# Performance work log

Hardware: AMD Instinct MI355X
Metric: run time of the kernel (lower is better)

## Reference

```python
import jax, jax.numpy as jnp
import numpy as np

N_HEAD = 16

def setup_inputs() -> dict:
    key = jax.random.key(0)
    ks = jax.random.split(key, 5)
    B, S, C = 4, 2048, 1024
    x = jax.random.normal(ks[0], (B, S, C), dtype=jnp.float32)
    w_qkv = jax.random.normal(ks[1], (C, 3 * C), dtype=jnp.float32) * (1.0 / np.sqrt(C))
    b_qkv = jnp.zeros((3 * C,), dtype=jnp.float32)
    w_proj = jax.random.normal(ks[2], (C, C), dtype=jnp.float32) * (1.0 / np.sqrt(C))
    b_proj = jnp.zeros((C,), dtype=jnp.float32)
    return {"x": x, "w_qkv": w_qkv, "b_qkv": b_qkv, "w_proj": w_proj, "b_proj": b_proj}

def reference(x, w_qkv, b_qkv, w_proj, b_proj):
    B, S, C = x.shape
    H = N_HEAD
    D = C // H
    qkv = x @ w_qkv + b_qkv                       # [B,S,3C]
    q, k, v = jnp.split(qkv, 3, axis=-1)
    # [B,S,C] -> [B,H,S,D]
    q = q.reshape(B, S, H, D).transpose(0, 2, 1, 3)
    k = k.reshape(B, S, H, D).transpose(0, 2, 1, 3)
    v = v.reshape(B, S, H, D).transpose(0, 2, 1, 3)
    scores = jnp.einsum('bhqd,bhkd->bhqk', q, k) / jnp.sqrt(jnp.float32(D))
    causal = jnp.tril(jnp.ones((S, S), dtype=bool))
    scores = jnp.where(causal[None, None], scores, -jnp.inf)
    weights = jax.nn.softmax(scores, axis=-1)     # dropout p=0 -> identity
    out = jnp.einsum('bhqk,bhkd->bhqd', weights, v)
    out = out.transpose(0, 2, 1, 3).reshape(B, S, C)
    return out @ w_proj + b_proj
```

## Files before the change

kernel.cpp:

```cpp
#include <hip/hip_runtime.h>

#define SDIM 2048
#define CDIM 1024
#define BDIM 4
#define HDIM 16
#define DDIM 64

#define ATT_SCALE 0.18033688011112042f

typedef __attribute__((ext_vector_type(8))) short bf16x8;
typedef __attribute__((ext_vector_type(4))) short bf16x4;
typedef __attribute__((ext_vector_type(4))) float f32x4;
typedef unsigned short u16;

#define MFMA __builtin_amdgcn_mfma_f32_16x16x32_bf16
#define LDS_ORDER_FENCE() __asm__ __volatile__("" ::: "memory")

__device__ __forceinline__ u16 f2b(float f) {
    union { float f; unsigned u; } v; v.f = f;
    unsigned r = v.u + 0x7FFFu + ((v.u >> 16) & 1u);
    return (u16)(r >> 16);
}
__device__ __forceinline__ u16 f2b_trunc(float f) {
    union { float f; unsigned u; } v; v.f = f;
    return (u16)(v.u >> 16);
}

typedef const __attribute__((address_space(1))) unsigned int* gas_t;
typedef __attribute__((address_space(3))) unsigned int* las_t;
__device__ __forceinline__ void cp16(const void* g, void* l) {
    __builtin_amdgcn_global_load_lds((gas_t)g, (las_t)l, 16, 0, 0);
}

__device__ __forceinline__ float fast_exp2(float x) {
#if __has_builtin(__builtin_amdgcn_exp2f)
    return __builtin_amdgcn_exp2f(x);
#else
    return __exp2f(x);
#endif
}

__global__ __launch_bounds__(256) void prep(
    const float* __restrict__ x, const float* __restrict__ w_qkv,
    const float* __restrict__ w_proj,
    u16* __restrict__ Xb, u16* __restrict__ WqT, u16* __restrict__ WpT)
{
    __shared__ __align__(16) u16 t[64][72];
    const int bx = blockIdx.x;
    const int tid = threadIdx.x;

    if (bx < 4096) {
        int i = (bx * 256 + tid) * 8;
        float4 a = *reinterpret_cast<const float4*>(&x[i]);
        float4 b = *reinterpret_cast<const float4*>(&x[i + 4]);
        u16 u[8];
        u[0]=f2b(a.x); u[1]=f2b(a.y); u[2]=f2b(a.z); u[3]=f2b(a.w);
        u[4]=f2b(b.x); u[5]=f2b(b.y); u[6]=f2b(b.z); u[7]=f2b(b.w);
        *reinterpret_cast<uint4*>(&Xb[i]) = *reinterpret_cast<uint4*>(u);
        return;
    }

    const float* src; u16* dst; int N, n0, k0;
    if (bx < 4096 + 768) {
        int b2 = bx - 4096;
        src = w_qkv; dst = WqT; N = 3 * CDIM;
        n0 = (b2 % 48) * 64; k0 = (b2 / 48) * 64;
    } else {
        int b2 = bx - 4864;
        src = w_proj; dst = WpT; N = CDIM;
        n0 = (b2 % 16) * 64; k0 = (b2 / 16) * 64;
    }
    const int K = CDIM;
#pragma unroll
    for (int it = 0; it < 4; it++) {
        int c = tid + it * 256;
        int r = c >> 4, c4 = (c & 15) * 4;
        float4 f = *reinterpret_cast<const float4*>(&src[(size_t)(k0 + r) * N + n0 + c4]);
        t[c4 + 0][r] = f2b(f.x);
        t[c4 + 1][r] = f2b(f.y);
        t[c4 + 2][r] = f2b(f.z);
        t[c4 + 3][r] = f2b(f.w);
    }
    __syncthreads();
#pragma unroll
    for (int it = 0; it < 2; it++) {
        int c = tid + it * 256;
        int r = c >> 3, c8 = (c & 7) * 8;
        *reinterpret_cast<uint4*>(&dst[(size_t)(n0 + r) * K + k0 + c8]) =
            *reinterpret_cast<const uint4*>(&t[r][c8]);
    }
}

#define PHASE_TAIL()                                                          \
    LDS_ORDER_FENCE();                                                        \
    __builtin_amdgcn_s_barrier();                                             \
    __asm__ __volatile__("s_waitcnt lgkmcnt(0)" ::: "memory");                \
    __builtin_amdgcn_sched_barrier(0)

#define PHASE_END()                                                           \
    LDS_ORDER_FENCE();                                                        \
    __builtin_amdgcn_s_barrier()

__global__ __launch_bounds__(256, 2) void gemm_qkv(
    const u16* __restrict__ A, const u16* __restrict__ Bt,
    const float* __restrict__ bias,
    u16* __restrict__ Qb, u16* __restrict__ Kb, u16* __restrict__ Vtb)
{
    __shared__ __align__(16) u16 smem[3 * 8192 + 3 * 4096];
    u16* const AsAll = smem;
    u16* const BsAll = smem + 3 * 8192;

    const int tid = threadIdx.x, lane = tid & 63, wave = tid >> 6;
    const int wm = wave >> 1, wn = wave & 1;
    const int l16 = lane & 15, quad = lane >> 4;
    const int bid = blockIdx.x;
    const int w = (bid & 7) * 96 + (bid >> 3);
    const int bx = w % 24, by = w / 24;
    const int m0 = by * 256, n0 = bx * 128;
    const int K = CDIM;

    const int su = (tid & 7) ^ ((tid >> 3) & 7);
    const int sr = ((tid >> 3) << 1) | (su >> 2);
    const int sc = su & 3;

    const int uc8 = ((((l16 & 1) << 2) | quad) ^ (l16 >> 1)) * 8;
    const int faB = (wm * 64 + (l16 >> 1)) * 64 + uc8;
    const int fbB = (wn * 32 + (l16 >> 1)) * 64 + uc8;

#define STG_A(sb, k0, s)  cp16(&A [(size_t)(m0 + (s) * 64 + sr) * K + (k0) + sc * 8], \
                               &AsAll[(sb) * 8192 + ((s) * 256 + wave * 64) * 8])
#define STG_B(sb, k0, s)  cp16(&Bt[(size_t)(n0 + (s) * 64 + sr) * K + (k0) + sc * 8], \
                               &BsAll[(sb) * 4096 + ((s) * 256 + wave * 64) * 8])
#define FRA(i) (*reinterpret_cast<const bf16x8*>(&AsB[faB + (i) * 512]))
#define FRB(j) (*reinterpret_cast<const bf16x8*>(&BsB[fbB + (j) * 512]))

    f32x4 acc[8][4];
#pragma unroll
    for (int i = 0; i < 8; i++)
#pragma unroll
        for (int j = 0; j < 4; j++) acc[i][j] = (f32x4){0.f, 0.f, 0.f, 0.f};

    const int NT = K / 32;
    STG_A(0, 0, 0); STG_A(0, 0, 1); STG_A(0, 0, 2); STG_A(0, 0, 3);
    STG_B(0, 0, 0); STG_B(0, 0, 1);
    STG_A(1, 32, 0); STG_A(1, 32, 1); STG_A(1, 32, 2); STG_A(1, 32, 3);
    STG_B(1, 32, 0); STG_B(1, 32, 1);
    __asm__ __volatile__("s_waitcnt vmcnt(6)" ::: "memory");
    __builtin_amdgcn_s_barrier();
    LDS_ORDER_FENCE();

    for (int t = 0; t < NT; t++) {
        const int buf = t % 3, sbuf = (t + 2) % 3;
        const int kst = (t + 2) * 32;
        const bool st = (t + 2) < NT;
        const u16* AsB = &AsAll[buf * 8192];
        const u16* BsB = &BsAll[buf * 4096];

        bf16x8 b0, b1, b2, b3, a0, a1, a2, a3;

        b0 = FRB(0); b1 = FRB(1); b2 = FRB(2); b3 = FRB(3);
        a0 = FRA(0); a1 = FRA(1); a2 = FRA(2); a3 = FRA(3);
        if (st) { STG_A(sbuf, kst, 0); STG_A(sbuf, kst, 1); STG_A(sbuf, kst, 2); }
        PHASE_TAIL();
        __builtin_amdgcn_s_setprio(1);
        acc[0][0] = MFMA(a0, b0, acc[0][0], 0, 0, 0);
        acc[0][1] = MFMA(a0, b1, acc[0][1], 0, 0, 0);
        acc[0][2] = MFMA(a0, b2, acc[0][2], 0, 0, 0);
        acc[0][3] = MFMA(a0, b3, acc[0][3], 0, 0, 0);
        acc[1][0] = MFMA(a1, b0, acc[1][0], 0, 0, 0);
        acc[1][1] = MFMA(a1, b1, acc[1][1], 0, 0, 0);
        acc[1][2] = MFMA(a1, b2, acc[1][2], 0, 0, 0);
        acc[1][3] = MFMA(a1, b3, acc[1][3], 0, 0, 0);
        acc[2][0] = MFMA(a2, b0, acc[2][0], 0, 0, 0);
        acc[2][1] = MFMA(a2, b1, acc[2][1], 0, 0, 0);
        acc[2][2] = MFMA(a2, b2, acc[2][2], 0, 0, 0);
        acc[2][3] = MFMA(a2, b3, acc[2][3], 0, 0, 0);
        acc[3][0] = MFMA(a3, b0, acc[3][0], 0, 0, 0);
        acc[3][1] = MFMA(a3, b1, acc[3][1], 0, 0, 0);
        acc[3][2] = MFMA(a3, b2, acc[3][2], 0, 0, 0);
        acc[3][3] = MFMA(a3, b3, acc[3][3], 0, 0, 0);
        __builtin_amdgcn_s_setprio(0);
        PHASE_END();

        a0 = FRA(4); a1 = FRA(5); a2 = FRA(6); a3 = FRA(7);
        if (st) { STG_A(sbuf, kst, 3); STG_B(sbuf, kst, 0); STG_B(sbuf, kst, 1); }
        PHASE_TAIL();
        __builtin_amdgcn_s_setprio(1);
        acc[4][0] = MFMA(a0, b0, acc[4][0], 0, 0, 0);
        acc[4][1] = MFMA(a0, b1, acc[4][1], 0, 0, 0);
        acc[4][2] = MFMA(a0, b2, acc[4][2], 0, 0, 0);
        acc[4][3] = MFMA(a0, b3, acc[4][3], 0, 0, 0);
        acc[5][0] = MFMA(a1, b0, acc[5][0], 0, 0, 0);
        acc[5][1] = MFMA(a1, b1, acc[5][1], 0, 0, 0);
        acc[5][2] = MFMA(a1, b2, acc[5][2], 0, 0, 0);
        acc[5][3] = MFMA(a1, b3, acc[5][3], 0, 0, 0);
        acc[6][0] = MFMA(a2, b0, acc[6][0], 0, 0, 0);
        acc[6][1] = MFMA(a2, b1, acc[6][1], 0, 0, 0);
        acc[6][2] = MFMA(a2, b2, acc[6][2], 0, 0, 0);
        acc[6][3] = MFMA(a2, b3, acc[6][3], 0, 0, 0);
        acc[7][0] = MFMA(a3, b0, acc[7][0], 0, 0, 0);
        acc[7][1] = MFMA(a3, b1, acc[7][1], 0, 0, 0);
        acc[7][2] = MFMA(a3, b2, acc[7][2], 0, 0, 0);
        acc[7][3] = MFMA(a3, b3, acc[7][3], 0, 0, 0);
        __builtin_amdgcn_s_setprio(0);
        if (t < NT - 2) {
            __asm__ __volatile__("s_waitcnt vmcnt(6)" ::: "memory");
        } else if (t == NT - 2) {
            __asm__ __volatile__("s_waitcnt vmcnt(0)" ::: "memory");
        }
        PHASE_END();
    }
#undef STG_A
#undef STG_B
#undef FRA
#undef FRB

    const int mm0 = m0 + wm * 128;
    const int bidx = mm0 >> 11, s0 = mm0 & 2047;
    const int n_base = n0 + wn * 64;
    u16* eb = &smem[wave * (16 * 68)];
    const int erow = lane >> 2, ec = (lane & 3) * 16;

    if (n0 >= 2 * CDIM) {
        const int h = (n_base - 2 * CDIM) >> 6;
        const size_t gb = ((size_t)(bidx * HDIM + h)) * DDIM * SDIM;
#pragma unroll
        for (int ih = 0; ih < 2; ih++) {
#pragma unroll
            for (int j = 0; j < 4; j++) {
                float bvj = bias[n_base + j * 16 + l16];
                LDS_ORDER_FENCE();
#pragma unroll
                for (int i = 0; i < 4; i++)
#pragma unroll
                    for (int r = 0; r < 4; r++)
                        eb[l16 * 68 + i * 16 + quad * 4 + r] =
                            f2b(acc[ih * 4 + i][j][r] + bvj);
                LDS_ORDER_FENCE();
                union { bf16x4 hp[4]; uint4 u[2]; } pk;
                pk.hp[0] = *reinterpret_cast<const bf16x4*>(&eb[erow * 68 + ec]);
                pk.hp[1] = *reinterpret_cast<const bf16x4*>(&eb[erow * 68 + ec + 4]);
                pk.hp[2] = *reinterpret_cast<const bf16x4*>(&eb[erow * 68 + ec + 8]);
                pk.hp[3] = *reinterpret_cast<const bf16x4*>(&eb[erow * 68 + ec + 12]);
                u16* gp = &Vtb[gb + (size_t)(j * 16 + erow) * SDIM + s0 + ih * 64 + ec];
                *reinterpret_cast<uint4*>(gp)     = pk.u[0];
                *reinterpret_cast<uint4*>(gp + 8) = pk.u[1];
            }
        }
    } else {
        const bool isK = (n_base >= CDIM);
        u16* dst = isK ? Kb : Qb;
        const float scale = isK ? 1.0f : ATT_SCALE;
        const int hh = (n_base & 1023) >> 6;
        const size_t hb = ((size_t)(bidx * HDIM + hh)) * SDIM;
        float bvj[4];
#pragma unroll
        for (int j = 0; j < 4; j++) bvj[j] = bias[n_base + j * 16 + l16];
#pragma unroll
        for (int i = 0; i < 8; i++) {
            LDS_ORDER_FENCE();
#pragma unroll
            for (int j = 0; j < 4; j++)
#pragma unroll
                for (int r = 0; r < 4; r++)
                    eb[(quad * 4 + r) * 68 + j * 16 + l16] =
                        f2b((acc[i][j][r] + bvj[j]) * scale);
            LDS_ORDER_FENCE();
            union { bf16x4 hp[4]; uint4 u[2]; } pk;
            pk.hp[0] = *reinterpret_cast<const bf16x4*>(&eb[erow * 68 + ec]);
            pk.hp[1] = *reinterpret_cast<const bf16x4*>(&eb[erow * 68 + ec + 4]);
            pk.hp[2] = *reinterpret_cast<const bf16x4*>(&eb[erow * 68 + ec + 8]);
            pk.hp[3] = *reinterpret_cast<const bf16x4*>(&eb[erow * 68 + ec + 12]);
            const int s = s0 + i * 16 + erow;
            u16* gp = &dst[(hb + s) * DDIM + ec];
            *reinterpret_cast<uint4*>(gp)     = pk.u[0];
            *reinterpret_cast<uint4*>(gp + 8) = pk.u[1];
        }
    }
}

__global__ __launch_bounds__(512, 6) void attn(
    const u16* __restrict__ Qb, const u16* __restrict__ Kb,
    const u16* __restrict__ Vtb, u16* __restrict__ Ob)
{
    __shared__ __align__(16) u16 Ks[2][64 * 64];
    __shared__ __align__(16) u16 Vts[2][64 * 64];
    __shared__ __align__(16) u16 Ps[8][16 * 68];

    const int tid = threadIdx.x;
    const int lane = tid & 63, wave = tid >> 6;
    const int l16 = lane & 15, quad = lane >> 4;
    const int x = blockIdx.x;
    const int bh = (x & 7) * 8 + ((x >> 3) & 7);
    const int qt = 15 - (x >> 6);
    const int q0 = qt * 128;
    const int b = bh >> 4, h = bh & 15;
    const size_t base = (size_t)bh * (SDIM * DDIM);

    const int cl0 = wave * 64 + lane;
    const int sr0 = cl0 >> 3, scc = cl0 & 7;
    const int sg0 = scc ^ (sr0 & 7);

    const int qrow = q0 + wave * 16 + l16;
    bf16x8 aq0 = *reinterpret_cast<const bf16x8*>(&Qb[base + (size_t)qrow * DDIM + quad * 8]);
    bf16x8 aq1 = *reinterpret_cast<const bf16x8*>(&Qb[base + (size_t)qrow * DDIM + 32 + quad * 8]);

    u16* Pw = &Ps[wave][0];

    f32x4 O[4];
    f32x4 Osum = (f32x4){0.f, 0.f, 0.f, 0.f};
#pragma unroll
    for (int j = 0; j < 4; j++) O[j] = (f32x4){0.f, 0.f, 0.f, 0.f};
    const short onev = (l16 == 0) ? (short)0x3F80 : (short)0;
    const bf16x8 bones = {onev, onev, onev, onev, onev, onev, onev, onev};

    const int nkb = (qt + 1) * 2;
    const int Arow = q0 + wave * 16;

    cp16(&Kb [base + (size_t)sr0 * DDIM + sg0 * 8], &Ks[0][wave * 512]);
    cp16(&Vtb[base + (size_t)sr0 * SDIM + sg0 * 8], &Vts[0][wave * 512]);

    for (int kbi = 0; kbi < nkb; kbi++) {
        const int cur = kbi & 1;
        const int kb = kbi * 64;
        __syncthreads();
        if (kbi + 1 < nkb) {
            const int kb2 = kb + 64;
            cp16(&Kb [base + (size_t)(kb2 + sr0) * DDIM + sg0 * 8], &Ks[1 - cur][wave * 512]);
            cp16(&Vtb[base + (size_t)sr0 * SDIM + kb2 + sg0 * 8], &Vts[1 - cur][wave * 512]);
        }
        if (kb > Arow + 15) continue;

        const u16* Kc = &Ks[cur][0];
        const u16* Vc = &Vts[cur][0];

        f32x4 sc[4];
#pragma unroll
        for (int j = 0; j < 4; j++) {
            int kr = j * 16 + l16;
            bf16x8 bk0 = *reinterpret_cast<const bf16x8*>(&Kc[(kr * 8 + ( quad      ^ (kr & 7))) * 8]);
            bf16x8 bk1 = *reinterpret_cast<const bf16x8*>(&Kc[(kr * 8 + ((quad + 4) ^ (kr & 7))) * 8]);
            f32x4 s = (f32x4){0.f, 0.f, 0.f, 0.f};
            s = MFMA(aq0, bk0, s, 0, 0, 0);
            s = MFMA(aq1, bk1, s, 0, 0, 0);
            sc[j] = s;
        }
        if (kb + 63 > Arow) {
            const int qrel = Arow - kb;
#pragma unroll
            for (int j = 0; j < 4; j++) {
                int kk = j * 16 + l16;
#pragma unroll
                for (int r = 0; r < 4; r++)
                    sc[j][r] = (kk <= qrel + quad * 4 + r) ? sc[j][r] : -1e30f;
            }
        }
#pragma unroll
        for (int j = 0; j < 4; j++)
#pragma unroll
            for (int r = 0; r < 4; r++) {
                float p = fast_exp2(sc[j][r]);
                Pw[(quad * 4 + r) * 68 + j * 16 + l16] = f2b_trunc(p);
            }
        LDS_ORDER_FENCE();
        union { bf16x4 hp[2]; bf16x8 f; } a0u, a1u;
        a0u.hp[0] = *reinterpret_cast<const bf16x4*>(&Pw[l16 * 68 + quad * 8]);
        a0u.hp[1] = *reinterpret_cast<const bf16x4*>(&Pw[l16 * 68 + quad * 8 + 4]);
        a1u.hp[0] = *reinterpret_cast<const bf16x4*>(&Pw[l16 * 68 + 32 + quad * 8]);
        a1u.hp[1] = *reinterpret_cast<const bf16x4*>(&Pw[l16 * 68 + 32 + quad * 8 + 4]);

#pragma unroll
        for (int j = 0; j < 4; j++) {
            int vr = j * 16 + l16;
            bf16x8 bv0 = *reinterpret_cast<const bf16x8*>(&Vc[(vr * 8 + ( quad      ^ (vr & 7))) * 8]);
            bf16x8 bv1 = *reinterpret_cast<const bf16x8*>(&Vc[(vr * 8 + ((quad + 4) ^ (vr & 7))) * 8]);
            O[j] = MFMA(a0u.f, bv0, O[j], 0, 0, 0);
            O[j] = MFMA(a1u.f, bv1, O[j], 0, 0, 0);
        }
        Osum = MFMA(a0u.f, bones, Osum, 0, 0, 0);
        Osum = MFMA(a1u.f, bones, Osum, 0, 0, 0);
    }

#pragma unroll
    for (int r = 0; r < 4; r++) {
        float l = __shfl(Osum[r], (lane & 48));
        float inv = 1.0f / l;
        int s = q0 + wave * 16 + quad * 4 + r;
#pragma unroll
        for (int j = 0; j < 4; j++)
            Ob[((size_t)(b * SDIM + s)) * CDIM + h * 64 + j * 16 + l16] =
                f2b(O[j][r] * inv);
    }
}

__global__ __launch_bounds__(512, 2) void gemm_proj(
    const u16* __restrict__ A, const u16* __restrict__ Bt,
    const float* __restrict__ bias, float* __restrict__ out)
{
    __shared__ __align__(16) u16 smem[3 * 16384 + 3 * 8192];
    u16* const AsAll = smem;
    u16* const BsAll = smem + 3 * 16384;

    const int tid = threadIdx.x, lane = tid & 63, wave = tid >> 6;
    const int wm = wave >> 1, wn = wave & 1;
    const int l16 = lane & 15, quad = lane >> 4;
    const int bid = blockIdx.x;
    const int w = (bid & 7) * 32 + (bid >> 3);
    const int bx = w & 7, by = w >> 3;
    const int m0 = by * 256, n0 = bx * 128;
    const int K = CDIM, N = CDIM;

    const int l8 = lane & 7, lr = lane >> 3;
    const int sg = l8 ^ lr;
    const int arow = wave * 8 + lr;

#define STG_A(sb, k0, s)  cp16(&A [(size_t)(m0 + (s) * 64 + arow) * K + (k0) + sg * 8], \
                               &AsAll[(sb) * 16384 + ((s) * 512 + wave * 64) * 8])
#define STG_B(sb, k0, s)  cp16(&Bt[(size_t)(n0 + (s) * 64 + arow) * K + (k0) + sg * 8], \
                               &BsAll[(sb) * 8192 + ((s) * 512 + wave * 64) * 8])
#define FRA(i, kk) (*reinterpret_cast<const bf16x8*>(                                   \
        &AsB[((wm * 64 + (i) * 16 + l16) * 8 + (((kk) * 4 + quad) ^ (l16 & 7))) * 8]))
#define FRB(j, kk) (*reinterpret_cast<const bf16x8*>(                                   \
        &BsB[((wn * 64 + (j) * 16 + l16) * 8 + (((kk) * 4 + quad) ^ (l16 & 7))) * 8]))

    f32x4 acc[4][4];
#pragma unroll
    for (int i = 0; i < 4; i++)
#pragma unroll
        for (int j = 0; j < 4; j++) acc[i][j] = (f32x4){0.f, 0.f, 0.f, 0.f};

    const int NT = K / 64;
    STG_A(0, 0, 0); STG_A(0, 0, 1); STG_A(0, 0, 2); STG_A(0, 0, 3);
    STG_B(0, 0, 0); STG_B(0, 0, 1);
    STG_A(1, 64, 0); STG_A(1, 64, 1); STG_A(1, 64, 2); STG_A(1, 64, 3);
    STG_B(1, 64, 0); STG_B(1, 64, 1);
    __asm__ __volatile__("s_waitcnt vmcnt(6)" ::: "memory");
    __builtin_amdgcn_s_barrier();
    LDS_ORDER_FENCE();

    for (int t = 0; t < NT; t++) {
        const int buf = t % 3, sbuf = (t + 2) % 3;
        const int kst = (t + 2) * 64;
        const bool st = (t + 2) < NT;
        const u16* AsB = &AsAll[buf * 16384];
        const u16* BsB = &BsAll[buf * 8192];

        bf16x8 b0, b1, b2, b3, a0, a1;

        b0 = FRB(0, 0); b1 = FRB(1, 0); b2 = FRB(2, 0); b3 = FRB(3, 0);
        a0 = FRA(0, 0); a1 = FRA(1, 0);
        if (st) { STG_A(sbuf, kst, 0); STG_A(sbuf, kst, 1); }
        PHASE_TAIL();
        __builtin_amdgcn_s_setprio(1);
        acc[0][0] = MFMA(a0, b0, acc[0][0], 0, 0, 0);
        acc[0][1] = MFMA(a0, b1, acc[0][1], 0, 0, 0);
        acc[0][2] = MFMA(a0, b2, acc[0][2], 0, 0, 0);
        acc[0][3] = MFMA(a0, b3, acc[0][3], 0, 0, 0);
        acc[1][0] = MFMA(a1, b0, acc[1][0], 0, 0, 0);
        acc[1][1] = MFMA(a1, b1, acc[1][1], 0, 0, 0);
        acc[1][2] = MFMA(a1, b2, acc[1][2], 0, 0, 0);
        acc[1][3] = MFMA(a1, b3, acc[1][3], 0, 0, 0);
        __builtin_amdgcn_s_setprio(0);
        PHASE_END();

        a0 = FRA(2, 0); a1 = FRA(3, 0);
        if (st) { STG_A(sbuf, kst, 2); STG_A(sbuf, kst, 3); }
        PHASE_TAIL();
        __builtin_amdgcn_s_setprio(1);
        acc[2][0] = MFMA(a0, b0, acc[2][0], 0, 0, 0);
        acc[2][1] = MFMA(a0, b1, acc[2][1], 0, 0, 0);
        acc[2][2] = MFMA(a0, b2, acc[2][2], 0, 0, 0);
        acc[2][3] = MFMA(a0, b3, acc[2][3], 0, 0, 0);
        acc[3][0] = MFMA(a1, b0, acc[3][0], 0, 0, 0);
        acc[3][1] = MFMA(a1, b1, acc[3][1], 0, 0, 0);
        acc[3][2] = MFMA(a1, b2, acc[3][2], 0, 0, 0);
        acc[3][3] = MFMA(a1, b3, acc[3][3], 0, 0, 0);
        __builtin_amdgcn_s_setprio(0);
        PHASE_END();

        b0 = FRB(0, 1); b1 = FRB(1, 1); b2 = FRB(2, 1); b3 = FRB(3, 1);
        a0 = FRA(0, 1); a1 = FRA(1, 1);
        if (st) { STG_B(sbuf, kst, 0); STG_B(sbuf, kst, 1); }
        PHASE_TAIL();
        __builtin_amdgcn_s_setprio(1);
        acc[0][0] = MFMA(a0, b0, acc[0][0], 0, 0, 0);
        acc[0][1] = MFMA(a0, b1, acc[0][1], 0, 0, 0);
        acc[0][2] = MFMA(a0, b2, acc[0][2], 0, 0, 0);
        acc[0][3] = MFMA(a0, b3, acc[0][3], 0, 0, 0);
        acc[1][0] = MFMA(a1, b0, acc[1][0], 0, 0, 0);
        acc[1][1] = MFMA(a1, b1, acc[1][1], 0, 0, 0);
        acc[1][2] = MFMA(a1, b2, acc[1][2], 0, 0, 0);
        acc[1][3] = MFMA(a1, b3, acc[1][3], 0, 0, 0);
        __builtin_amdgcn_s_setprio(0);
        PHASE_END();

        a0 = FRA(2, 1); a1 = FRA(3, 1);
        PHASE_TAIL();
        __builtin_amdgcn_s_setprio(1);
        acc[2][0] = MFMA(a0, b0, acc[2][0], 0, 0, 0);
        acc[2][1] = MFMA(a0, b1, acc[2][1], 0, 0, 0);
        acc[2][2] = MFMA(a0, b2, acc[2][2], 0, 0, 0);
        acc[2][3] = MFMA(a0, b3, acc[2][3], 0, 0, 0);
        acc[3][0] = MFMA(a1, b0, acc[3][0], 0, 0, 0);
        acc[3][1] = MFMA(a1, b1, acc[3][1], 0, 0, 0);
        acc[3][2] = MFMA(a1, b2, acc[3][2], 0, 0, 0);
        acc[3][3] = MFMA(a1, b3, acc[3][3], 0, 0, 0);
        __builtin_amdgcn_s_setprio(0);
        if (t < NT - 2) {
            __asm__ __volatile__("s_waitcnt vmcnt(6)" ::: "memory");
        } else if (t == NT - 2) {
            __asm__ __volatile__("s_waitcnt vmcnt(0)" ::: "memory");
        }
        PHASE_END();
    }
#undef STG_A
#undef STG_B
#undef FRA
#undef FRB

#pragma unroll
    for (int i = 0; i < 4; i++) {
        int mbase = m0 + wm * 64 + i * 16 + quad * 4;
#pragma unroll
        for (int j = 0; j < 4; j++) {
            int n = n0 + wn * 64 + j * 16 + l16;
            float bv = bias[n];
#pragma unroll
            for (int r = 0; r < 4; r++)
                out[(size_t)(mbase + r) * N + n] = acc[i][j][r] + bv;
        }
    }
}

extern "C" void kernel_launch(void* const* d_in, const int* in_sizes, int n_in,
                              void* d_out, int out_size, void* d_ws, size_t ws_size,
                              hipStream_t stream) {
    const float* x      = (const float*)d_in[0];
    const float* w_qkv  = (const float*)d_in[1];
    const float* b_qkv  = (const float*)d_in[2];
    const float* w_proj = (const float*)d_in[3];
    const float* b_proj = (const float*)d_in[4];
    float* out = (float*)d_out;

    const size_t per = (size_t)BDIM * HDIM * SDIM * DDIM;
    u16* Qb  = (u16*)d_ws;
    u16* Kb  = Qb + per;
    u16* Vtb = Kb + per;
    u16* Ob  = Vtb + per;
    u16* Xb  = Ob;
    u16* WqT = Ob + per;
    u16* WpT = WqT + (size_t)3 * CDIM * CDIM;

    prep<<<dim3(4096 + 768 + 256), dim3(256), 0, stream>>>(x, w_qkv, w_proj, Xb, WqT, WpT);

    gemm_qkv<<<dim3(768), dim3(256), 0, stream>>>(Xb, WqT, b_qkv, Qb, Kb, Vtb);
    attn<<<dim3(BDIM * HDIM * (SDIM / 128)), dim3(512), 0, stream>>>(Qb, Kb, Vtb, Ob);
    gemm_proj<<<dim3(256), dim3(512), 0, stream>>>(Ob, WpT, b_proj, out);
}
```

Baseline: 232.7 us.

## Double attention query tile per wave to reuse K/V fragments across two row groups

Each wave now handles 32 query rows (two 16-row MFMA groups) instead of 16, so the block covers 256 queries and each K/V LDS fragment feeds twice as many MFMAs. The grid halves to 512 blocks. The query-tile order is reworked so the first 256 blocks take heavy tiles in descending order and the rest take light tiles ascending, which spreads causal work more evenly. This costs more registers and LDS for P, lowers occupancy (launch bounds 6 to 4), and means fewer blocks to balance across CUs.

```diff
diff --git a/kernel.cpp b/kernel.cpp
--- a/kernel.cpp
+++ b/kernel.cpp
@@ -279,21 +279,22 @@
     }
 }
 
-__global__ __launch_bounds__(512, 6) void attn(
+__global__ __launch_bounds__(512, 4) void attn(
     const u16* __restrict__ Qb, const u16* __restrict__ Kb,
     const u16* __restrict__ Vtb, u16* __restrict__ Ob)
 {
     __shared__ __align__(16) u16 Ks[2][64 * 64];
     __shared__ __align__(16) u16 Vts[2][64 * 64];
-    __shared__ __align__(16) u16 Ps[8][16 * 68];
+    __shared__ __align__(16) u16 Ps[8][32 * 68];
 
     const int tid = threadIdx.x;
     const int lane = tid & 63, wave = tid >> 6;
     const int l16 = lane & 15, quad = lane >> 4;
     const int x = blockIdx.x;
     const int bh = (x & 7) * 8 + ((x >> 3) & 7);
-    const int qt = 15 - (x >> 6);
-    const int q0 = qt * 128;
+    const int g8 = (x >> 6) & 3;
+    const int qt = (x >> 8) ? g8 : (7 - g8);
+    const int q0 = qt * 256;
     const int b = bh >> 4, h = bh & 15;
     const size_t base = (size_t)bh * (SDIM * DDIM);
 
@@ -301,21 +302,28 @@
     const int sr0 = cl0 >> 3, scc = cl0 & 7;
     const int sg0 = scc ^ (sr0 & 7);
 
-    const int qrow = q0 + wave * 16 + l16;
-    bf16x8 aq0 = *reinterpret_cast<const bf16x8*>(&Qb[base + (size_t)qrow * DDIM + quad * 8]);
-    bf16x8 aq1 = *reinterpret_cast<const bf16x8*>(&Qb[base + (size_t)qrow * DDIM + 32 + quad * 8]);
+    const int qr0 = q0 + wave * 32 + l16;
+    bf16x8 aq0 = *reinterpret_cast<const bf16x8*>(&Qb[base + (size_t)qr0 * DDIM + quad * 8]);
+    bf16x8 aq1 = *reinterpret_cast<const bf16x8*>(&Qb[base + (size_t)qr0 * DDIM + 32 + quad * 8]);
+    const int qr1 = qr0 + 16;
+    bf16x8 aq2 = *reinterpret_cast<const bf16x8*>(&Qb[base + (size_t)qr1 * DDIM + quad * 8]);
+    bf16x8 aq3 = *reinterpret_cast<const bf16x8*>(&Qb[base + (size_t)qr1 * DDIM + 32 + quad * 8]);
 
     u16* Pw = &Ps[wave][0];
 
-    f32x4 O[4];
-    f32x4 Osum = (f32x4){0.f, 0.f, 0.f, 0.f};
-#pragma unroll
-    for (int j = 0; j < 4; j++) O[j] = (f32x4){0.f, 0.f, 0.f, 0.f};
+    f32x4 O[2][4];
+    f32x4 Osum[2];
+#pragma unroll
+    for (int g = 0; g < 2; g++) {
+        Osum[g] = (f32x4){0.f, 0.f, 0.f, 0.f};
+#pragma unroll
+        for (int j = 0; j < 4; j++) O[g][j] = (f32x4){0.f, 0.f, 0.f, 0.f};
+    }
     const short onev = (l16 == 0) ? (short)0x3F80 : (short)0;
     const bf16x8 bones = {onev, onev, onev, onev, onev, onev, onev, onev};
 
-    const int nkb = (qt + 1) * 2;
-    const int Arow = q0 + wave * 16;
+    const int nkb = (qt + 1) * 4;
+    const int Arow = q0 + wave * 32;
 
     cp16(&Kb [base + (size_t)sr0 * DDIM + sg0 * 8], &Ks[0][wave * 512]);
     cp16(&Vtb[base + (size_t)sr0 * SDIM + sg0 * 8], &Vts[0][wave * 512]);
@@ -329,12 +337,12 @@
             cp16(&Kb [base + (size_t)(kb2 + sr0) * DDIM + sg0 * 8], &Ks[1 - cur][wave * 512]);
             cp16(&Vtb[base + (size_t)sr0 * SDIM + kb2 + sg0 * 8], &Vts[1 - cur][wave * 512]);
         }
-        if (kb > Arow + 15) continue;
+        if (kb > Arow + 31) continue;
 
         const u16* Kc = &Ks[cur][0];
         const u16* Vc = &Vts[cur][0];
 
-        f32x4 sc[4];
+        f32x4 sc0[4], sc1[4];
 #pragma unroll
         for (int j = 0; j < 4; j++) {
             int kr = j * 16 + l16;
@@ -343,53 +351,70 @@
             f32x4 s = (f32x4){0.f, 0.f, 0.f, 0.f};
             s = MFMA(aq0, bk0, s, 0, 0, 0);
             s = MFMA(aq1, bk1, s, 0, 0, 0);
-            sc[j] = s;
+            sc0[j] = s;
+            s = (f32x4){0.f, 0.f, 0.f, 0.f};
+            s = MFMA(aq2, bk0, s, 0, 0, 0);
+            s = MFMA(aq3, bk1, s, 0, 0, 0);
+            sc1[j] = s;
         }
         if (kb + 63 > Arow) {
-            const int qrel = Arow - kb;
+            const int qrel0 = Arow - kb;
 #pragma unroll
             for (int j = 0; j < 4; j++) {
                 int kk = j * 16 + l16;
 #pragma unroll
-                for (int r = 0; r < 4; r++)
-                    sc[j][r] = (kk <= qrel + quad * 4 + r) ? sc[j][r] : -1e30f;
+                for (int r = 0; r < 4; r++) {
+                    sc0[j][r] = (kk <= qrel0 + quad * 4 + r)      ? sc0[j][r] : -1e30f;
+                    sc1[j][r] = (kk <= qrel0 + 16 + quad * 4 + r) ? sc1[j][r] : -1e30f;
+                }
             }
         }
 #pragma unroll
         for (int j = 0; j < 4; j++)
 #pragma unroll
             for (int r = 0; r < 4; r++) {
-                float p = fast_exp2(sc[j][r]);
-                Pw[(quad * 4 + r) * 68 + j * 16 + l16] = f2b_trunc(p);
+                Pw[(quad * 4 + r) * 68 + j * 16 + l16]        = f2b_trunc(fast_exp2(sc0[j][r]));
+                Pw[(16 + quad * 4 + r) * 68 + j * 16 + l16]   = f2b_trunc(fast_exp2(sc1[j][r]));
             }
         LDS_ORDER_FENCE();
-        union { bf16x4 hp[2]; bf16x8 f; } a0u, a1u;
+        union { bf16x4 hp[2]; bf16x8 f; } a0u, a1u, a2u, a3u;
         a0u.hp[0] = *reinterpret_cast<const bf16x4*>(&Pw[l16 * 68 + quad * 8]);
         a0u.hp[1] = *reinterpret_cast<const bf16x4*>(&Pw[l16 * 68 + quad * 8 + 4]);
         a1u.hp[0] = *reinterpret_cast<const bf16x4*>(&Pw[l16 * 68 + 32 + quad * 8]);
         a1u.hp[1] = *reinterpret_cast<const bf16x4*>(&Pw[l16 * 68 + 32 + quad * 8 + 4]);
+        a2u.hp[0] = *reinterpret_cast<const bf16x4*>(&Pw[(16 + l16) * 68 + quad * 8]);
+        a2u.hp[1] = *reinterpret_cast<const bf16x4*>(&Pw[(16 + l16) * 68 + quad * 8 + 4]);
+        a3u.hp[0] = *reinterpret_cast<const bf16x4*>(&Pw[(16 + l16) * 68 + 32 + quad * 8]);
+        a3u.hp[1] = *reinterpret_cast<const bf16x4*>(&Pw[(16 + l16) * 68 + 32 + quad * 8 + 4]);
 
 #pragma unroll
         for (int j = 0; j < 4; j++) {
             int vr = j * 16 + l16;
             bf16x8 bv0 = *reinterpret_cast<const bf16x8*>(&Vc[(vr * 8 + ( quad      ^ (vr & 7))) * 8]);
             bf16x8 bv1 = *reinterpret_cast<const bf16x8*>(&Vc[(vr * 8 + ((quad + 4) ^ (vr & 7))) * 8]);
-            O[j] = MFMA(a0u.f, bv0, O[j], 0, 0, 0);
-            O[j] = MFMA(a1u.f, bv1, O[j], 0, 0, 0);
-        }
-        Osum = MFMA(a0u.f, bones, Osum, 0, 0, 0);
-        Osum = MFMA(a1u.f, bones, Osum, 0, 0, 0);
-    }
-
-#pragma unroll
-    for (int r = 0; r < 4; r++) {
-        float l = __shfl(Osum[r], (lane & 48));
-        float inv = 1.0f / l;
-        int s = q0 + wave * 16 + quad * 4 + r;
-#pragma unroll
-        for (int j = 0; j < 4; j++)
-            Ob[((size_t)(b * SDIM + s)) * CDIM + h * 64 + j * 16 + l16] =
-                f2b(O[j][r] * inv);
+            O[0][j] = MFMA(a0u.f, bv0, O[0][j], 0, 0, 0);
+            O[0][j] = MFMA(a1u.f, bv1, O[0][j], 0, 0, 0);
+            O[1][j] = MFMA(a2u.f, bv0, O[1][j], 0, 0, 0);
+            O[1][j] = MFMA(a3u.f, bv1, O[1][j], 0, 0, 0);
+        }
+        Osum[0] = MFMA(a0u.f, bones, Osum[0], 0, 0, 0);
+        Osum[0] = MFMA(a1u.f, bones, Osum[0], 0, 0, 0);
+        Osum[1] = MFMA(a2u.f, bones, Osum[1], 0, 0, 0);
+        Osum[1] = MFMA(a3u.f, bones, Osum[1], 0, 0, 0);
+    }
+
+#pragma unroll
+    for (int g = 0; g < 2; g++) {
+#pragma unroll
+        for (int r = 0; r < 4; r++) {
+            float l = __shfl(Osum[g][r], (lane & 48));
+            float inv = 1.0f / l;
+            int s = q0 + wave * 32 + g * 16 + quad * 4 + r;
+#pragma unroll
+            for (int j = 0; j < 4; j++)
+                Ob[((size_t)(b * SDIM + s)) * CDIM + h * 64 + j * 16 + l16] =
+                    f2b(O[g][j][r] * inv);
+        }
     }
 }
 
@@ -554,6 +579,6 @@
     prep<<<dim3(4096 + 768 + 256), dim3(256), 0, stream>>>(x, w_qkv, w_proj, Xb, WqT, WpT);
 
     gemm_qkv<<<dim3(768), dim3(256), 0, stream>>>(Xb, WqT, b_qkv, Qb, Kb, Vtb);
-    attn<<<dim3(BDIM * HDIM * (SDIM / 128)), dim3(512), 0, stream>>>(Qb, Kb, Vtb, Ob);
+    attn<<<dim3(512), dim3(512), 0, stream>>>(Qb, Kb, Vtb, Ob);
     gemm_proj<<<dim3(256), dim3(512), 0, stream>>>(Ob, WpT, b_proj, out);
 }
```

Result: no change. 234.1 us (+0.6%).
